# Kernel optimization log

Hardware: AMD Instinct MI355X
Metric: run time of the kernel (lower is better)

## Reference

```python
import jax, jax.numpy as jnp
import numpy as np

N = 100000
E = 1600000
IN_C, HID_C, OUT_C = 64, 64, 16


def setup_inputs() -> dict:
    key = jax.random.key(0)
    k1, k2, k3, k4, k5 = jax.random.split(key, 5)
    x = jax.random.normal(k1, (N, IN_C), dtype=jnp.float32)
    edge_index = jax.random.randint(k2, (2, E), 0, N, dtype=jnp.int64)
    # Glorot-style init like PyG GCNConv
    W1 = jax.random.normal(k3, (IN_C, HID_C), dtype=jnp.float32) * (1.0 / np.sqrt(IN_C))
    b1 = jnp.zeros((HID_C,), dtype=jnp.float32)
    W2 = jax.random.normal(k4, (HID_C, OUT_C), dtype=jnp.float32) * (1.0 / np.sqrt(HID_C))
    b2 = jnp.zeros((OUT_C,), dtype=jnp.float32)
    return {"x": x, "edge_index": edge_index, "W1": W1, "b1": b1, "W2": W2, "b2": b2}


def _gcn_conv(h, src, dst, norm, W, b, n_nodes):
    # h: [N, F_in] -> linear transform first (PyG order), then normalized aggregation
    h = h @ W  # [N, F_out]
    msgs = h[src] * norm[:, None]          # gather + scale, [E+N, F_out]
    out = jax.ops.segment_sum(msgs, dst, num_segments=n_nodes)  # scatter-add
    return out + b


def reference(x, edge_index, W1, b1, W2, b2):
    n = x.shape[0]
    loop = jnp.arange(n, dtype=edge_index.dtype)
    src = jnp.concatenate([edge_index[0], loop])  # add self-loops
    dst = jnp.concatenate([edge_index[1], loop])
    # symmetric normalization D^{-1/2} (A+I) D^{-1/2}
    deg = jax.ops.segment_sum(jnp.ones_like(dst, dtype=x.dtype), dst, num_segments=n)
    dinv = jnp.where(deg > 0, jax.lax.rsqrt(deg), 0.0)
    norm = dinv[src] * dinv[dst]  # [E+N]

    h = jax.nn.relu(_gcn_conv(x, src, dst, norm, W1, b1, n))
    # dropout is identity in eval mode
    return _gcn_conv(h, src, dst, norm, W2, b2, n)
```

## Files before the change

kernel.cpp:

```cpp
#include <hip/hip_runtime.h>


namespace {
constexpr int BLK = 256;
constexpr int NPB = 256;
constexpr int PCHUNK = 8192;
constexpr int STRIDE = 5120;
constexpr int CPAD = 32;

__device__ inline float bf2f(unsigned short h) {
    union { unsigned u; float f; } v; v.u = (unsigned)h << 16; return v.f;
}
__device__ inline unsigned short f2bf(float f) {
    union { float f; unsigned u; } v; v.f = f;
    unsigned r = (v.u + 0x7FFFu + ((v.u >> 16) & 1u)) >> 16;
    return (unsigned short)r;
}
__device__ inline unsigned pack2bf(float a, float b) {
    return (unsigned)f2bf(a) | ((unsigned)f2bf(b) << 16);
}
__device__ inline int sel4(int s0, int s1, int s2, int s3, int q) {
    int sa = (q & 1) ? s1 : s0;
    int sb = (q & 1) ? s3 : s2;
    return (q & 2) ? sb : sa;
}

__device__ inline float gather8(const unsigned short* __restrict__ hhat,
                                const int* __restrict__ ssrc, int base, int lane) {
    int s0 = ssrc[base + 0], s1 = ssrc[base + 1];
    int s2 = ssrc[base + 2], s3 = ssrc[base + 3];
    int s4 = ssrc[base + 4], s5 = ssrc[base + 5];
    int s6 = ssrc[base + 6], s7 = ssrc[base + 7];
    float v0 = bf2f(hhat[((size_t)s0 << 6) + lane]);
    float v1 = bf2f(hhat[((size_t)s1 << 6) + lane]);
    float v2 = bf2f(hhat[((size_t)s2 << 6) + lane]);
    float v3 = bf2f(hhat[((size_t)s3 << 6) + lane]);
    float v4 = bf2f(hhat[((size_t)s4 << 6) + lane]);
    float v5 = bf2f(hhat[((size_t)s5 << 6) + lane]);
    float v6 = bf2f(hhat[((size_t)s6 << 6) + lane]);
    float v7 = bf2f(hhat[((size_t)s7 << 6) + lane]);
    return ((v0 + v1) + (v2 + v3)) + ((v4 + v5) + (v6 + v7));
}
__device__ inline float gather4(const unsigned short* __restrict__ hhat,
                                const int* __restrict__ ssrc, int base, int lane) {
    int s0 = ssrc[base + 0], s1 = ssrc[base + 1];
    int s2 = ssrc[base + 2], s3 = ssrc[base + 3];
    float v0 = bf2f(hhat[((size_t)s0 << 6) + lane]);
    float v1 = bf2f(hhat[((size_t)s1 << 6) + lane]);
    float v2 = bf2f(hhat[((size_t)s2 << 6) + lane]);
    float v3 = bf2f(hhat[((size_t)s3 << 6) + lane]);
    return (v0 + v1) + (v2 + v3);
}

__global__ __launch_bounds__(BLK) void k_zero(int* __restrict__ p, int n) {
    int i = blockIdx.x * BLK + threadIdx.x;
    if (i < n) p[i] = 0;
}

__global__ __launch_bounds__(BLK) void k_part(const int* __restrict__ src,
                                              const int* __restrict__ dst,
                                              int* __restrict__ bcnt,
                                              unsigned* __restrict__ packed,
                                              int e, int nb) {
    __shared__ int hist[1024];
    __shared__ int base[1024];
    int t = threadIdx.x;
    int chunk0 = blockIdx.x * PCHUNK;
    if (chunk0 >= e) return;
    int lim = min(PCHUNK, e - chunk0);
    int lim4 = lim >> 2;
    for (int i = t; i < nb; i += BLK) hist[i] = 0;
    __syncthreads();
    const int4* d4 = (const int4*)(dst + chunk0);
    for (int i = t; i < lim4; i += BLK) {
        int4 d = d4[i];
        atomicAdd(&hist[d.x >> 8], 1);
        atomicAdd(&hist[d.y >> 8], 1);
        atomicAdd(&hist[d.z >> 8], 1);
        atomicAdd(&hist[d.w >> 8], 1);
    }
    for (int i = (lim4 << 2) + t; i < lim; i += BLK)
        atomicAdd(&hist[dst[chunk0 + i] >> 8], 1);
    __syncthreads();
    for (int i = t; i < nb; i += BLK) {
        int c = hist[i];
        base[i] = c ? (i * STRIDE + atomicAdd(&bcnt[i * CPAD], c)) : 0;
        hist[i] = 0;
    }
    __syncthreads();
    const int4* s4 = (const int4*)(src + chunk0);
    for (int i = t; i < lim4; i += BLK) {
        int4 d = d4[i];
        int4 s = s4[i];
        int b0 = d.x >> 8, b1 = d.y >> 8, b2 = d.z >> 8, b3 = d.w >> 8;
        int r0 = atomicAdd(&hist[b0], 1);
        packed[base[b0] + r0] = ((unsigned)s.x << 8) | (unsigned)(d.x & 255);
        int r1 = atomicAdd(&hist[b1], 1);
        packed[base[b1] + r1] = ((unsigned)s.y << 8) | (unsigned)(d.y & 255);
        int r2 = atomicAdd(&hist[b2], 1);
        packed[base[b2] + r2] = ((unsigned)s.z << 8) | (unsigned)(d.z & 255);
        int r3 = atomicAdd(&hist[b3], 1);
        packed[base[b3] + r3] = ((unsigned)s.w << 8) | (unsigned)(d.w & 255);
    }
    for (int i = (lim4 << 2) + t; i < lim; i += BLK) {
        int d = dst[chunk0 + i];
        int b = d >> 8;
        int r = atomicAdd(&hist[b], 1);
        packed[base[b] + r] = ((unsigned)src[chunk0 + i] << 8) | (unsigned)(d & 255);
    }
}

__global__ __launch_bounds__(512) void k_sort(const unsigned* __restrict__ packed,
                                              const int* __restrict__ bcnt,
                                              int* __restrict__ ssrc,
                                              int* __restrict__ rowbeg,
                                              int* __restrict__ rowcnt,
                                              float* __restrict__ dinv, int n) {
    __shared__ unsigned sp[STRIDE];
    __shared__ int cnt[NPB];
    __shared__ int offs[NPB];
    int b = blockIdx.x;
    int t = threadIdx.x;
    int regionBase = b * STRIDE;
    int ecnt = bcnt[b * CPAD];
    if (t < NPB) cnt[t] = 0;
    __syncthreads();
    for (int i = t; i < ecnt; i += 512) {
        unsigned p = packed[regionBase + i];
        sp[i] = p;
        atomicAdd(&cnt[p & 255u], 1);
    }
    __syncthreads();
    if (t < NPB) offs[t] = cnt[t];
    __syncthreads();
    for (int off = 1; off < NPB; off <<= 1) {
        int x = 0;
        if (t < NPB && t >= off) x = offs[t - off];
        __syncthreads();
        if (t < NPB) offs[t] += x;
        __syncthreads();
    }
    int myoff = 0;
    if (t < NPB) {
        int v = cnt[t];
        myoff = offs[t] - v;
        int node = (b << 8) + t;
        if (node < n) {
            rowbeg[node] = regionBase + myoff;
            rowcnt[node] = v;
            dinv[node] = rsqrtf((float)(v + 1));
        }
    }
    __syncthreads();
    if (t < NPB) cnt[t] = regionBase + myoff;
    __syncthreads();
    for (int i = t; i < ecnt; i += 512) {
        unsigned p = sp[i];
        int pos = atomicAdd(&cnt[p & 255u], 1);
        ssrc[pos] = (int)(p >> 8);
    }
}


__global__ __launch_bounds__(BLK) void k_gemm1(const float* __restrict__ x,
                                               const float* __restrict__ W1,
                                               const float* __restrict__ dinv,
                                               unsigned short* __restrict__ hhat, int n) {
    __shared__ float W[64 * 64];
    int t = threadIdx.x;
    #pragma unroll
    for (int i = 0; i < 16; ++i) W[t + BLK * i] = W1[t + BLK * i];
    __syncthreads();
    const int cg = t & 3;
    const int ng = t >> 2;
    const int node0 = blockIdx.x * 256 + ng * 4;
    const float* Wc = W + cg * 16;

    int nd[4];
    #pragma unroll
    for (int i = 0; i < 4; ++i) {
        int v = node0 + i;
        nd[i] = (v < n) ? v : (n - 1);
    }

    float4 acc[4][4];
    #pragma unroll
    for (int i = 0; i < 4; ++i)
        #pragma unroll
        for (int c = 0; c < 4; ++c) acc[i][c] = make_float4(0.f, 0.f, 0.f, 0.f);

    for (int k4 = 0; k4 < 16; ++k4) {
        float4 xv[4];
        #pragma unroll
        for (int i = 0; i < 4; ++i)
            xv[i] = ((const float4*)(x + (size_t)nd[i] * 64))[k4];
        #pragma unroll
        for (int kk = 0; kk < 4; ++kk) {
            const float4* wr = (const float4*)(Wc + (k4 * 4 + kk) * 64);
            float4 w0 = wr[0], w1 = wr[1], w2 = wr[2], w3 = wr[3];
            #pragma unroll
            for (int i = 0; i < 4; ++i) {
                float xa[4] = {xv[i].x, xv[i].y, xv[i].z, xv[i].w};
                float xs = xa[kk];
                acc[i][0].x = fmaf(xs, w0.x, acc[i][0].x);
                acc[i][0].y = fmaf(xs, w0.y, acc[i][0].y);
                acc[i][0].z = fmaf(xs, w0.z, acc[i][0].z);
                acc[i][0].w = fmaf(xs, w0.w, acc[i][0].w);
                acc[i][1].x = fmaf(xs, w1.x, acc[i][1].x);
                acc[i][1].y = fmaf(xs, w1.y, acc[i][1].y);
                acc[i][1].z = fmaf(xs, w1.z, acc[i][1].z);
                acc[i][1].w = fmaf(xs, w1.w, acc[i][1].w);
                acc[i][2].x = fmaf(xs, w2.x, acc[i][2].x);
                acc[i][2].y = fmaf(xs, w2.y, acc[i][2].y);
                acc[i][2].z = fmaf(xs, w2.z, acc[i][2].z);
                acc[i][2].w = fmaf(xs, w2.w, acc[i][2].w);
                acc[i][3].x = fmaf(xs, w3.x, acc[i][3].x);
                acc[i][3].y = fmaf(xs, w3.y, acc[i][3].y);
                acc[i][3].z = fmaf(xs, w3.z, acc[i][3].z);
                acc[i][3].w = fmaf(xs, w3.w, acc[i][3].w);
            }
        }
    }
    #pragma unroll
    for (int i = 0; i < 4; ++i) {
        int v = node0 + i;
        if (v < n) {
            float d = dinv[v];
            unsigned u0 = pack2bf(acc[i][0].x * d, acc[i][0].y * d);
            unsigned u1 = pack2bf(acc[i][0].z * d, acc[i][0].w * d);
            unsigned u2 = pack2bf(acc[i][1].x * d, acc[i][1].y * d);
            unsigned u3 = pack2bf(acc[i][1].z * d, acc[i][1].w * d);
            unsigned u4 = pack2bf(acc[i][2].x * d, acc[i][2].y * d);
            unsigned u5 = pack2bf(acc[i][2].z * d, acc[i][2].w * d);
            unsigned u6 = pack2bf(acc[i][3].x * d, acc[i][3].y * d);
            unsigned u7 = pack2bf(acc[i][3].z * d, acc[i][3].w * d);
            uint4* dst = (uint4*)(hhat + (size_t)v * 64 + cg * 16);
            dst[0] = make_uint4(u0, u1, u2, u3);
            dst[1] = make_uint4(u4, u5, u6, u7);
        }
    }
}

__global__ __launch_bounds__(BLK) void k_agg1(const unsigned short* __restrict__ hhat,
                                              const int* __restrict__ rowbeg,
                                              const int* __restrict__ rowcnt,
                                              const int* __restrict__ ssrc,
                                              const float* __restrict__ dinv,
                                              const float* __restrict__ b1,
                                              const float* __restrict__ W2,
                                              unsigned short* __restrict__ h2hat, int n) {
    int pair = __builtin_amdgcn_readfirstlane(
        (int)((blockIdx.x * BLK + threadIdx.x) >> 6));
    int lane = threadIdx.x & 63;
    int wid0 = pair << 1;
    if (wid0 >= n) return;
    int wid1 = wid0 + 1;
    bool has1 = (wid1 < n);
    const int g = lane >> 4;
    const int j = lane & 15;
    float w2r[16];
    #pragma unroll
    for (int k = 0; k < 16; ++k) w2r[k] = W2[(g * 16 + k) * 16 + j];

    int beg0 = rowbeg[wid0], cnt0 = rowcnt[wid0];
    int beg1 = 0, cnt1 = 0;
    if (has1) { beg1 = rowbeg[wid1]; cnt1 = rowcnt[wid1]; }
    float a0 = bf2f(hhat[((size_t)wid0 << 6) + lane]);
    float a1 = 0.f;
    if (has1) a1 = bf2f(hhat[((size_t)wid1 << 6) + lane]);
    int e0 = 0, e1 = 0;
    while (e0 + 8 <= cnt0 && e1 + 8 <= cnt1) {
        float r0 = gather8(hhat, ssrc, beg0 + e0, lane);
        float r1 = gather8(hhat, ssrc, beg1 + e1, lane);
        a0 += r0;
        a1 += r1;
        e0 += 8; e1 += 8;
    }
    for (; e0 + 8 <= cnt0; e0 += 8) a0 += gather8(hhat, ssrc, beg0 + e0, lane);
    for (; e1 + 8 <= cnt1; e1 += 8) a1 += gather8(hhat, ssrc, beg1 + e1, lane);
    if (e0 + 4 <= cnt0) { a0 += gather4(hhat, ssrc, beg0 + e0, lane); e0 += 4; }
    if (e1 + 4 <= cnt1) { a1 += gather4(hhat, ssrc, beg1 + e1, lane); e1 += 4; }
    for (; e0 < cnt0; ++e0) a0 += bf2f(hhat[((size_t)ssrc[beg0 + e0] << 6) + lane]);
    for (; e1 < cnt1; ++e1) a1 += bf2f(hhat[((size_t)ssrc[beg1 + e1] << 6) + lane]);

    {
        float dv = dinv[wid0];
        float h = fmaxf(fmaf(dv, a0, b1[lane]), 0.f);
        float part = 0.f;
        #pragma unroll
        for (int k = 0; k < 16; ++k)
            part = fmaf(__shfl(h, g * 16 + k, 64), w2r[k], part);
        part += __shfl_xor(part, 16, 64);
        part += __shfl_xor(part, 32, 64);
        if (g == 0) h2hat[(size_t)wid0 * 16 + j] = f2bf(part * dv);
    }
    if (has1) {
        float dv = dinv[wid1];
        float h = fmaxf(fmaf(dv, a1, b1[lane]), 0.f);
        float part = 0.f;
        #pragma unroll
        for (int k = 0; k < 16; ++k)
            part = fmaf(__shfl(h, g * 16 + k, 64), w2r[k], part);
        part += __shfl_xor(part, 16, 64);
        part += __shfl_xor(part, 32, 64);
        if (g == 0) h2hat[(size_t)wid1 * 16 + j] = f2bf(part * dv);
    }
}

__global__ __launch_bounds__(BLK) void k_agg2(const unsigned short* __restrict__ h2,
                                              const int* __restrict__ rowbeg,
                                              const int* __restrict__ rowcnt,
                                              const int* __restrict__ ssrc,
                                              const float* __restrict__ dinv,
                                              const float* __restrict__ b2,
                                              float* __restrict__ out, int n) {
    int pair = __builtin_amdgcn_readfirstlane(
        (int)((blockIdx.x * BLK + threadIdx.x) >> 6));
    int lane = threadIdx.x & 63;
    int w0 = pair << 1;
    if (w0 >= n) return;
    int w1 = w0 + 1;
    bool has1 = (w1 < n);
    int q = lane >> 4;
    int c = lane & 15;
    int beg0 = rowbeg[w0], cnt0 = rowcnt[w0];
    int beg1 = 0, cnt1 = 0;
    if (has1) { beg1 = rowbeg[w1]; cnt1 = rowcnt[w1]; }
    float a0 = 0.f, a1 = 0.f;
    int e0 = 0, e1 = 0;
    while (e0 + 8 <= cnt0 && e1 + 8 <= cnt1) {
        int p0 = beg0 + e0, p1 = beg1 + e1;
        int x0 = ssrc[p0 + 0], x1 = ssrc[p0 + 1], x2 = ssrc[p0 + 2], x3 = ssrc[p0 + 3];
        int x4 = ssrc[p0 + 4], x5 = ssrc[p0 + 5], x6 = ssrc[p0 + 6], x7 = ssrc[p0 + 7];
        int y0 = ssrc[p1 + 0], y1 = ssrc[p1 + 1], y2 = ssrc[p1 + 2], y3 = ssrc[p1 + 3];
        int y4 = ssrc[p1 + 4], y5 = ssrc[p1 + 5], y6 = ssrc[p1 + 6], y7 = ssrc[p1 + 7];
        int sA0 = sel4(x0, x1, x2, x3, q), sB0 = sel4(x4, x5, x6, x7, q);
        int sA1 = sel4(y0, y1, y2, y3, q), sB1 = sel4(y4, y5, y6, y7, q);
        float vA0 = bf2f(h2[((size_t)sA0 << 4) + c]);
        float vB0 = bf2f(h2[((size_t)sB0 << 4) + c]);
        float vA1 = bf2f(h2[((size_t)sA1 << 4) + c]);
        float vB1 = bf2f(h2[((size_t)sB1 << 4) + c]);
        a0 += vA0 + vB0;
        a1 += vA1 + vB1;
        e0 += 8; e1 += 8;
    }
    for (; e0 + 8 <= cnt0; e0 += 8) {
        int p0 = beg0 + e0;
        int x0 = ssrc[p0 + 0], x1 = ssrc[p0 + 1], x2 = ssrc[p0 + 2], x3 = ssrc[p0 + 3];
        int x4 = ssrc[p0 + 4], x5 = ssrc[p0 + 5], x6 = ssrc[p0 + 6], x7 = ssrc[p0 + 7];
        int sA = sel4(x0, x1, x2, x3, q), sB = sel4(x4, x5, x6, x7, q);
        a0 += bf2f(h2[((size_t)sA << 4) + c]) + bf2f(h2[((size_t)sB << 4) + c]);
    }
    if (e0 + 4 <= cnt0) {
        int p0 = beg0 + e0;
        int x0 = ssrc[p0 + 0], x1 = ssrc[p0 + 1], x2 = ssrc[p0 + 2], x3 = ssrc[p0 + 3];
        a0 += bf2f(h2[((size_t)sel4(x0, x1, x2, x3, q) << 4) + c]);
        e0 += 4;
    }
    if (e0 + q < cnt0)
        a0 += bf2f(h2[((size_t)ssrc[beg0 + e0 + q] << 4) + c]);
    for (; e1 + 8 <= cnt1; e1 += 8) {
        int p1 = beg1 + e1;
        int y0 = ssrc[p1 + 0], y1 = ssrc[p1 + 1], y2 = ssrc[p1 + 2], y3 = ssrc[p1 + 3];
        int y4 = ssrc[p1 + 4], y5 = ssrc[p1 + 5], y6 = ssrc[p1 + 6], y7 = ssrc[p1 + 7];
        int sA = sel4(y0, y1, y2, y3, q), sB = sel4(y4, y5, y6, y7, q);
        a1 += bf2f(h2[((size_t)sA << 4) + c]) + bf2f(h2[((size_t)sB << 4) + c]);
    }
    if (has1 && e1 + 4 <= cnt1) {
        int p1 = beg1 + e1;
        int y0 = ssrc[p1 + 0], y1 = ssrc[p1 + 1], y2 = ssrc[p1 + 2], y3 = ssrc[p1 + 3];
        a1 += bf2f(h2[((size_t)sel4(y0, y1, y2, y3, q) << 4) + c]);
        e1 += 4;
    }
    if (has1 && e1 + q < cnt1)
        a1 += bf2f(h2[((size_t)ssrc[beg1 + e1 + q] << 4) + c]);

    a0 += __shfl_xor(a0, 16, 64);
    a0 += __shfl_xor(a0, 32, 64);
    a1 += __shfl_xor(a1, 16, 64);
    a1 += __shfl_xor(a1, 32, 64);
    if (q == 0) {
        float self0 = bf2f(h2[((size_t)w0 << 4) + c]);
        out[((size_t)w0 << 4) + c] = fmaf(dinv[w0], a0 + self0, b2[c]);
        if (has1) {
            float self1 = bf2f(h2[((size_t)w1 << 4) + c]);
            out[((size_t)w1 << 4) + c] = fmaf(dinv[w1], a1 + self1, b2[c]);
        }
    }
}

}

extern "C" void kernel_launch(void* const* d_in, const int* in_sizes, int n_in,
                              void* d_out, int out_size, void* d_ws, size_t ws_size,
                              hipStream_t stream) {
    const float* x  = (const float*)d_in[0];
    const int*   ei = (const int*)d_in[1];
    const float* W1 = (const float*)d_in[2];
    const float* b1 = (const float*)d_in[3];
    const float* W2 = (const float*)d_in[4];
    const float* b2 = (const float*)d_in[5];
    float* out = (float*)d_out;

    const int N = in_sizes[0] / 64;
    const int E = in_sizes[1] / 2;
    const int* src = ei;
    const int* dst = ei + E;
    const int nb = (N + NPB - 1) / NPB;

    char* ws = (char*)d_ws;
    size_t off = 0;
    auto alloc = [&](size_t bytes) -> char* {
        char* p = ws + off;
        off = (off + bytes + 255) & ~(size_t)255;
        return p;
    };
    int*            bcnt   = (int*)alloc((size_t)1024 * CPAD * 4);
    int*            rowbeg = (int*)alloc((size_t)N * 4);
    int*            rowcnt = (int*)alloc((size_t)N * 4);
    float*          dinv   = (float*)alloc((size_t)N * 4);
    unsigned*       packed = (unsigned*)alloc((size_t)nb * STRIDE * 4);
    int*            ssrc   = (int*)alloc((size_t)nb * STRIDE * 4);
    unsigned short* hhat   = (unsigned short*)alloc((size_t)N * 64 * 2);
    unsigned short* h2hat  = (unsigned short*)alloc((size_t)N * 16 * 2);

    const int nb_n = (N + BLK - 1) / BLK;
    const int nchunks = (E + PCHUNK - 1) / PCHUNK;
    const int npairs = (N + 1) / 2;
    const int nb_p = (int)(((long long)npairs * 64 + BLK - 1) / BLK);

    const int zn = nb * CPAD;
    k_zero<<<(zn + BLK - 1) / BLK, BLK, 0, stream>>>(bcnt, zn);
    k_part<<<nchunks, BLK, 0, stream>>>(src, dst, bcnt, packed, E, nb);
    k_sort<<<nb, 512, 0, stream>>>(packed, bcnt, ssrc, rowbeg, rowcnt, dinv, N);

    k_gemm1<<<nb_n, BLK, 0, stream>>>(x, W1, dinv, hhat, N);
    k_agg1<<<nb_p, BLK, 0, stream>>>(hhat, rowbeg, rowcnt, ssrc, dinv, b1, W2,
                                     h2hat, N);
    k_agg2<<<nb_p, BLK, 0, stream>>>(h2hat, rowbeg, rowcnt, ssrc, dinv, b2, out, N);
}
```

Baseline: 210.8 us.

## Split bucket sort across four blocks per bucket and persist-loop gemm1 tiles

k_sort now launches four 256-thread blocks per 256-node bucket instead of one 512-thread block. Each block redundantly loads and histograms the whole bucket, then writes only the rows and edges for its own quarter of destination nodes. This raises parallelism for the small grid of about 391 blocks, at the cost of four times the bucket reads and histogram atomics. k_gemm1 becomes a grid-stride loop over node tiles with the grid capped at 1024, which amortizes the W1 shared-memory load; with only 391 tiles the cap never binds, so that part changes little.

```diff
diff --git a/kernel.cpp b/kernel.cpp
--- a/kernel.cpp
+++ b/kernel.cpp
@@ -110,7 +110,7 @@
     }
 }
 
-__global__ __launch_bounds__(512) void k_sort(const unsigned* __restrict__ packed,
+__global__ __launch_bounds__(BLK) void k_sort(const unsigned* __restrict__ packed,
                                               const int* __restrict__ bcnt,
                                               int* __restrict__ ssrc,
                                               int* __restrict__ rowbeg,
@@ -119,45 +119,47 @@
     __shared__ unsigned sp[STRIDE];
     __shared__ int cnt[NPB];
     __shared__ int offs[NPB];
-    int b = blockIdx.x;
+    int bid = blockIdx.x;
+    int b = bid >> 2;
+    int qr = bid & 3;
     int t = threadIdx.x;
     int regionBase = b * STRIDE;
     int ecnt = bcnt[b * CPAD];
-    if (t < NPB) cnt[t] = 0;
-    __syncthreads();
-    for (int i = t; i < ecnt; i += 512) {
+    cnt[t] = 0;
+    __syncthreads();
+    for (int i = t; i < ecnt; i += BLK) {
         unsigned p = packed[regionBase + i];
         sp[i] = p;
         atomicAdd(&cnt[p & 255u], 1);
     }
     __syncthreads();
-    if (t < NPB) offs[t] = cnt[t];
+    int v = cnt[t];
+    offs[t] = v;
     __syncthreads();
     for (int off = 1; off < NPB; off <<= 1) {
-        int x = 0;
-        if (t < NPB && t >= off) x = offs[t - off];
+        int x = (t >= off) ? offs[t - off] : 0;
         __syncthreads();
-        if (t < NPB) offs[t] += x;
+        offs[t] += x;
         __syncthreads();
     }
-    int myoff = 0;
-    if (t < NPB) {
-        int v = cnt[t];
-        myoff = offs[t] - v;
-        int node = (b << 8) + t;
-        if (node < n) {
-            rowbeg[node] = regionBase + myoff;
-            rowcnt[node] = v;
-            dinv[node] = rsqrtf((float)(v + 1));
+    int myoff = offs[t] - v;
+    int node = (b << 8) + t;
+    if ((t >> 6) == qr && node < n) {
+        rowbeg[node] = regionBase + myoff;
+        rowcnt[node] = v;
+        dinv[node] = rsqrtf((float)(v + 1));
+    }
+    __syncthreads();
+    cnt[t] = regionBase + myoff;
+    __syncthreads();
+    int lo = qr << 6, hi = lo + 64;
+    for (int i = t; i < ecnt; i += BLK) {
+        unsigned p = sp[i];
+        int dl = (int)(p & 255u);
+        if (dl >= lo && dl < hi) {
+            int pos = atomicAdd(&cnt[dl], 1);
+            ssrc[pos] = (int)(p >> 8);
         }
-    }
-    __syncthreads();
-    if (t < NPB) cnt[t] = regionBase + myoff;
-    __syncthreads();
-    for (int i = t; i < ecnt; i += 512) {
-        unsigned p = sp[i];
-        int pos = atomicAdd(&cnt[p & 255u], 1);
-        ssrc[pos] = (int)(p >> 8);
     }
 }
 
@@ -165,7 +167,8 @@
 __global__ __launch_bounds__(BLK) void k_gemm1(const float* __restrict__ x,
                                                const float* __restrict__ W1,
                                                const float* __restrict__ dinv,
-                                               unsigned short* __restrict__ hhat, int n) {
+                                               unsigned short* __restrict__ hhat,
+                                               int n, int ntiles) {
     __shared__ float W[64 * 64];
     int t = threadIdx.x;
     #pragma unroll
@@ -173,70 +176,71 @@
     __syncthreads();
     const int cg = t & 3;
     const int ng = t >> 2;
-    const int node0 = blockIdx.x * 256 + ng * 4;
     const float* Wc = W + cg * 16;
 
-    int nd[4];
-    #pragma unroll
-    for (int i = 0; i < 4; ++i) {
-        int v = node0 + i;
-        nd[i] = (v < n) ? v : (n - 1);
-    }
-
-    float4 acc[4][4];
-    #pragma unroll
-    for (int i = 0; i < 4; ++i)
+    for (int tile = blockIdx.x; tile < ntiles; tile += gridDim.x) {
+        const int node0 = tile * 256 + ng * 4;
+        int nd[4];
         #pragma unroll
-        for (int c = 0; c < 4; ++c) acc[i][c] = make_float4(0.f, 0.f, 0.f, 0.f);
-
-    for (int k4 = 0; k4 < 16; ++k4) {
-        float4 xv[4];
+        for (int i = 0; i < 4; ++i) {
+            int v = node0 + i;
+            nd[i] = (v < n) ? v : (n - 1);
+        }
+        float4 acc[4][4];
         #pragma unroll
         for (int i = 0; i < 4; ++i)
-            xv[i] = ((const float4*)(x + (size_t)nd[i] * 64))[k4];
-        #pragma unroll
-        for (int kk = 0; kk < 4; ++kk) {
-            const float4* wr = (const float4*)(Wc + (k4 * 4 + kk) * 64);
-            float4 w0 = wr[0], w1 = wr[1], w2 = wr[2], w3 = wr[3];
             #pragma unroll
-            for (int i = 0; i < 4; ++i) {
-                float xa[4] = {xv[i].x, xv[i].y, xv[i].z, xv[i].w};
-                float xs = xa[kk];
-                acc[i][0].x = fmaf(xs, w0.x, acc[i][0].x);
-                acc[i][0].y = fmaf(xs, w0.y, acc[i][0].y);
-                acc[i][0].z = fmaf(xs, w0.z, acc[i][0].z);
-                acc[i][0].w = fmaf(xs, w0.w, acc[i][0].w);
-                acc[i][1].x = fmaf(xs, w1.x, acc[i][1].x);
-                acc[i][1].y = fmaf(xs, w1.y, acc[i][1].y);
-                acc[i][1].z = fmaf(xs, w1.z, acc[i][1].z);
-                acc[i][1].w = fmaf(xs, w1.w, acc[i][1].w);
-                acc[i][2].x = fmaf(xs, w2.x, acc[i][2].x);
-                acc[i][2].y = fmaf(xs, w2.y, acc[i][2].y);
-                acc[i][2].z = fmaf(xs, w2.z, acc[i][2].z);
-                acc[i][2].w = fmaf(xs, w2.w, acc[i][2].w);
-                acc[i][3].x = fmaf(xs, w3.x, acc[i][3].x);
-                acc[i][3].y = fmaf(xs, w3.y, acc[i][3].y);
-                acc[i][3].z = fmaf(xs, w3.z, acc[i][3].z);
-                acc[i][3].w = fmaf(xs, w3.w, acc[i][3].w);
+            for (int c = 0; c < 4; ++c) acc[i][c] = make_float4(0.f, 0.f, 0.f, 0.f);
+
+        for (int k4 = 0; k4 < 16; ++k4) {
+            float4 xv[4];
+            #pragma unroll
+            for (int i = 0; i < 4; ++i)
+                xv[i] = ((const float4*)(x + (size_t)nd[i] * 64))[k4];
+            #pragma unroll
+            for (int kk = 0; kk < 4; ++kk) {
+                const float4* wr = (const float4*)(Wc + (k4 * 4 + kk) * 64);
+                float4 w0 = wr[0], w1 = wr[1], w2 = wr[2], w3 = wr[3];
+                #pragma unroll
+                for (int i = 0; i < 4; ++i) {
+                    float xa[4] = {xv[i].x, xv[i].y, xv[i].z, xv[i].w};
+                    float xs = xa[kk];
+                    acc[i][0].x = fmaf(xs, w0.x, acc[i][0].x);
+                    acc[i][0].y = fmaf(xs, w0.y, acc[i][0].y);
+                    acc[i][0].z = fmaf(xs, w0.z, acc[i][0].z);
+                    acc[i][0].w = fmaf(xs, w0.w, acc[i][0].w);
+                    acc[i][1].x = fmaf(xs, w1.x, acc[i][1].x);
+                    acc[i][1].y = fmaf(xs, w1.y, acc[i][1].y);
+                    acc[i][1].z = fmaf(xs, w1.z, acc[i][1].z);
+                    acc[i][1].w = fmaf(xs, w1.w, acc[i][1].w);
+                    acc[i][2].x = fmaf(xs, w2.x, acc[i][2].x);
+                    acc[i][2].y = fmaf(xs, w2.y, acc[i][2].y);
+                    acc[i][2].z = fmaf(xs, w2.z, acc[i][2].z);
+                    acc[i][2].w = fmaf(xs, w2.w, acc[i][2].w);
+                    acc[i][3].x = fmaf(xs, w3.x, acc[i][3].x);
+                    acc[i][3].y = fmaf(xs, w3.y, acc[i][3].y);
+                    acc[i][3].z = fmaf(xs, w3.z, acc[i][3].z);
+                    acc[i][3].w = fmaf(xs, w3.w, acc[i][3].w);
+                }
             }
         }
-    }
-    #pragma unroll
-    for (int i = 0; i < 4; ++i) {
-        int v = node0 + i;
-        if (v < n) {
-            float d = dinv[v];
-            unsigned u0 = pack2bf(acc[i][0].x * d, acc[i][0].y * d);
-            unsigned u1 = pack2bf(acc[i][0].z * d, acc[i][0].w * d);
-            unsigned u2 = pack2bf(acc[i][1].x * d, acc[i][1].y * d);
-            unsigned u3 = pack2bf(acc[i][1].z * d, acc[i][1].w * d);
-            unsigned u4 = pack2bf(acc[i][2].x * d, acc[i][2].y * d);
-            unsigned u5 = pack2bf(acc[i][2].z * d, acc[i][2].w * d);
-            unsigned u6 = pack2bf(acc[i][3].x * d, acc[i][3].y * d);
-            unsigned u7 = pack2bf(acc[i][3].z * d, acc[i][3].w * d);
-            uint4* dst = (uint4*)(hhat + (size_t)v * 64 + cg * 16);
-            dst[0] = make_uint4(u0, u1, u2, u3);
-            dst[1] = make_uint4(u4, u5, u6, u7);
+        #pragma unroll
+        for (int i = 0; i < 4; ++i) {
+            int v = node0 + i;
+            if (v < n) {
+                float d = dinv[v];
+                unsigned u0 = pack2bf(acc[i][0].x * d, acc[i][0].y * d);
+                unsigned u1 = pack2bf(acc[i][0].z * d, acc[i][0].w * d);
+                unsigned u2 = pack2bf(acc[i][1].x * d, acc[i][1].y * d);
+                unsigned u3 = pack2bf(acc[i][1].z * d, acc[i][1].w * d);
+                unsigned u4 = pack2bf(acc[i][2].x * d, acc[i][2].y * d);
+                unsigned u5 = pack2bf(acc[i][2].z * d, acc[i][2].w * d);
+                unsigned u6 = pack2bf(acc[i][3].x * d, acc[i][3].y * d);
+                unsigned u7 = pack2bf(acc[i][3].z * d, acc[i][3].w * d);
+                uint4* dst = (uint4*)(hhat + (size_t)v * 64 + cg * 16);
+                dst[0] = make_uint4(u0, u1, u2, u3);
+                dst[1] = make_uint4(u4, u5, u6, u7);
+            }
         }
     }
 }
@@ -424,7 +428,8 @@
     unsigned short* hhat   = (unsigned short*)alloc((size_t)N * 64 * 2);
     unsigned short* h2hat  = (unsigned short*)alloc((size_t)N * 16 * 2);
 
-    const int nb_n = (N + BLK - 1) / BLK;
+    const int ntiles = (N + 255) / 256;
+    const int g1grid = (ntiles < 1024) ? ntiles : 1024;
     const int nchunks = (E + PCHUNK - 1) / PCHUNK;
     const int npairs = (N + 1) / 2;
     const int nb_p = (int)(((long long)npairs * 64 + BLK - 1) / BLK);
@@ -432,9 +437,9 @@
     const int zn = nb * CPAD;
     k_zero<<<(zn + BLK - 1) / BLK, BLK, 0, stream>>>(bcnt, zn);
     k_part<<<nchunks, BLK, 0, stream>>>(src, dst, bcnt, packed, E, nb);
-    k_sort<<<nb, 512, 0, stream>>>(packed, bcnt, ssrc, rowbeg, rowcnt, dinv, N);
-
-    k_gemm1<<<nb_n, BLK, 0, stream>>>(x, W1, dinv, hhat, N);
+    k_sort<<<nb * 4, BLK, 0, stream>>>(packed, bcnt, ssrc, rowbeg, rowcnt, dinv, N);
+
+    k_gemm1<<<g1grid, BLK, 0, stream>>>(x, W1, dinv, hhat, N, ntiles);
     k_agg1<<<nb_p, BLK, 0, stream>>>(hhat, rowbeg, rowcnt, ssrc, dinv, b1, W2,
                                      h2hat, N);
     k_agg2<<<nb_p, BLK, 0, stream>>>(h2hat, rowbeg, rowcnt, ssrc, dinv, b2, out, N);
```

After: 200.1 us. -5.1%, faster.
